# Kernel tuning notes

Measured on AMD Instinct MI355X. Metric: run time of the kernel, lower is better.

## Reference

```python
import jax, jax.numpy as jnp
import numpy as np

B, N, DIN, DM, NH = 8, 2048, 256, 256, 4
DK = DM // NH


def setup_inputs() -> dict:
    key = jax.random.key(0)
    ks = jax.random.split(key, 8)
    x = jax.random.normal(ks[0], (B, N, DIN), dtype=jnp.float32)
    # contiguous valid ranges per sample (padding on both ends), matching
    # the module's assumption that torch.where(mask)[0][0]/[−1] define a span
    starts = jax.random.randint(ks[1], (B,), 0, N // 8)
    lens = jax.random.randint(ks[2], (B,), N // 2, N - N // 8)
    pos = jnp.arange(N)
    attention_mask = ((pos[None, :] >= starts[:, None])
                      & (pos[None, :] < starts[:, None] + lens[:, None])).astype(jnp.int32)
    s = 0.02
    Wq = jax.random.normal(ks[3], (DIN, DM), jnp.float32) * s
    Wk = jax.random.normal(ks[4], (DIN, DM), jnp.float32) * s
    Wv = jax.random.normal(ks[5], (DIN, DM), jnp.float32) * s
    Wo = jax.random.normal(ks[6], (DM, DM), jnp.float32) * s
    bq = jnp.zeros((DM,), jnp.float32)
    bk = jnp.zeros((DM,), jnp.float32)
    bv = jnp.zeros((DM,), jnp.float32)
    bo = jnp.zeros((DM,), jnp.float32)
    return {"x": x, "attention_mask": attention_mask,
            "Wq": Wq, "bq": bq, "Wk": Wk, "bk": bk,
            "Wv": Wv, "bv": bv, "Wo": Wo, "bo": bo}


def reference(x, attention_mask, Wq, bq, Wk, bk, Wv, bv, Wo, bo):
    b, n, _ = x.shape
    nh, dk = NH, DK
    scale = 1.0 / np.sqrt(dk)
    q = (x @ Wq + bq).reshape(b, n, nh, dk).transpose(0, 2, 1, 3)  # [b,h,n,dk]
    k = (x @ Wk + bk).reshape(b, n, nh, dk).transpose(0, 2, 1, 3)
    v = (x @ Wv + bv).reshape(b, n, nh, dk).transpose(0, 2, 1, 3)
    dist = jnp.einsum('bhid,bhjd->bhij', q, k) * scale  # [b,h,n,n]

    # Vectorized equivalent of the per-sample python-loop mask:
    # start = first True index; end = last True index (torch slice start:end
    # is EXCLUSIVE of the last valid position -- preserved faithfully).
    m = attention_mask.astype(bool)
    pos = jnp.arange(n)
    start = jnp.argmax(m, axis=1)                      # [b]
    end = n - 1 - jnp.argmax(m[:, ::-1], axis=1)       # [b] last True index
    valid = (pos[None, :] >= start[:, None]) & (pos[None, :] < end[:, None])  # [b,n]
    bias = jnp.where(valid[:, :, None] & valid[:, None, :], 0.0, -1e10)       # [b,n,n]

    dist = jax.nn.softmax(dist + bias[:, None, :, :], axis=-1)
    att = jnp.einsum('bhij,bhjd->bhid', dist, v)       # [b,h,n,dk]
    att = att.transpose(0, 2, 1, 3).reshape(b, n, nh * dk)
    return att @ Wo + bo
```

## Files before the change

kernel.cpp:

```cpp
#include <hip/hip_runtime.h>
#include <hip/hip_bf16.h>
#include <math.h>

namespace {
constexpr int Bb  = 8;
constexpr int Nn  = 2048;
constexpr int DIN_ = 256;
constexpr int DM_  = 256;
constexpr int NH_  = 4;
constexpr int DK_  = 64;
constexpr int BH_  = Bb * NH_;
constexpr float SCALE = 0.125f;
}

typedef __attribute__((ext_vector_type(8))) _Float16 half8;
typedef __attribute__((ext_vector_type(2))) __fp16 fp16x2;
typedef __attribute__((ext_vector_type(4))) float f32x4;

static __device__ __forceinline__ unsigned pkrtz_u32(float a, float b) {
    union { fp16x2 h; unsigned u; } u;
    u.h = __builtin_amdgcn_cvt_pkrtz(a, b);
    return u.u;
}

static __device__ __forceinline__ half8 h8_from_u32x4(unsigned w0, unsigned w1,
                                                      unsigned w2, unsigned w3) {
    union { unsigned u[4]; half8 h; } u;
    u.u[0] = w0; u.u[1] = w1; u.u[2] = w2; u.u[3] = w3;
    return u.h;
}

__global__ __launch_bounds__(256) void bounds_kernel(const int* __restrict__ mask,
                                                     int* __restrict__ bounds) {
    const int b = blockIdx.x;
    const int tid = threadIdx.x;
    __shared__ int smin[256], smax[256];
    int lmin = Nn, lmax = -1;
    for (int i = tid; i < Nn; i += 256) {
        if (mask[b * Nn + i]) {
            if (i < lmin) lmin = i;
            if (i > lmax) lmax = i;
        }
    }
    smin[tid] = lmin; smax[tid] = lmax;
    __syncthreads();
    for (int s = 128; s > 0; s >>= 1) {
        if (tid < s) {
            smin[tid] = min(smin[tid], smin[tid + s]);
            smax[tid] = max(smax[tid], smax[tid + s]);
        }
        __syncthreads();
    }
    if (tid == 0) { bounds[b * 2] = smin[0]; bounds[b * 2 + 1] = smax[0]; }
}

__global__ __launch_bounds__(256) void convert_x(const float* __restrict__ x,
                                                 _Float16* __restrict__ xh) {
    const size_t i = ((size_t)blockIdx.x * 256 + threadIdx.x) * 8;
    float4 v0 = *(const float4*)&x[i];
    float4 v1 = *(const float4*)&x[i + 4];
    _Float16 h[8];
    h[0]=(_Float16)v0.x; h[1]=(_Float16)v0.y; h[2]=(_Float16)v0.z; h[3]=(_Float16)v0.w;
    h[4]=(_Float16)v1.x; h[5]=(_Float16)v1.y; h[6]=(_Float16)v1.z; h[7]=(_Float16)v1.w;
    *(uint4*)&xh[i] = *(const uint4*)h;
}

__global__ __launch_bounds__(256) void convert_w(
    const float* __restrict__ W0, const float* __restrict__ W1,
    const float* __restrict__ W2, const float* __restrict__ W3,
    _Float16* __restrict__ T0, _Float16* __restrict__ T1,
    _Float16* __restrict__ T2, _Float16* __restrict__ T3)
{
    const float* W; _Float16* T;
    switch (blockIdx.y) {
        case 0: W = W0; T = T0; break;
        case 1: W = W1; T = T1; break;
        case 2: W = W2; T = T2; break;
        default: W = W3; T = T3; break;
    }
    const int idx = blockIdx.x * 256 + threadIdx.x;
    const int n = idx & 255;
    const int k0 = (idx >> 8) << 2;
    _Float16 h4[4];
    #pragma unroll
    for (int j = 0; j < 4; ++j) h4[j] = (_Float16)W[(size_t)(k0 + j) * 256 + n];
    *(uint2*)&T[(size_t)n * 256 + k0] = *(const uint2*)h4;
}

__global__ __launch_bounds__(256) void qkv_mfma(
    const _Float16* __restrict__ xh,
    const _Float16* __restrict__ Wtq, const float* __restrict__ bq,
    const _Float16* __restrict__ Wtk, const float* __restrict__ bk,
    const _Float16* __restrict__ Wtv, const float* __restrict__ bv,
    _Float16* __restrict__ Qh, _Float16* __restrict__ Kh, _Float16* __restrict__ Vt)
{
    const int z = blockIdx.z;
    const _Float16* Wt; const float* bias;
    if (z == 0)      { Wt = Wtq; bias = bq; }
    else if (z == 1) { Wt = Wtk; bias = bk; }
    else             { Wt = Wtv; bias = bv; }

    const int m0 = blockIdx.x * 128;
    const int n0 = blockIdx.y * 64;
    const int tid = threadIdx.x;
    const int w = tid >> 6, lane = tid & 63;
    const int a = lane & 15, g = lane >> 4;
    const int mb = m0 + 32 * w;

    f32x4 d0[4] = {{0,0,0,0},{0,0,0,0},{0,0,0,0},{0,0,0,0}};
    f32x4 d1[4] = {{0,0,0,0},{0,0,0,0},{0,0,0,0},{0,0,0,0}};

    const _Float16* A0 = xh + (size_t)(mb + a) * 256 + 8 * g;
    const _Float16* A1 = xh + (size_t)(mb + 16 + a) * 256 + 8 * g;
    const _Float16* Wr0 = Wt + (size_t)(n0 +  0 + a) * 256 + 8 * g;
    const _Float16* Wr1 = Wt + (size_t)(n0 + 16 + a) * 256 + 8 * g;
    const _Float16* Wr2 = Wt + (size_t)(n0 + 32 + a) * 256 + 8 * g;
    const _Float16* Wr3 = Wt + (size_t)(n0 + 48 + a) * 256 + 8 * g;

    #pragma unroll
    for (int kc = 0; kc < 8; ++kc) {
        const half8 af0 = *(const half8*)(A0 + 32 * kc);
        const half8 af1 = *(const half8*)(A1 + 32 * kc);
        const half8 b0 = *(const half8*)(Wr0 + 32 * kc);
        const half8 b1 = *(const half8*)(Wr1 + 32 * kc);
        const half8 b2 = *(const half8*)(Wr2 + 32 * kc);
        const half8 b3 = *(const half8*)(Wr3 + 32 * kc);
        d0[0] = __builtin_amdgcn_mfma_f32_16x16x32_f16(af0, b0, d0[0], 0,0,0);
        d1[0] = __builtin_amdgcn_mfma_f32_16x16x32_f16(af1, b0, d1[0], 0,0,0);
        d0[1] = __builtin_amdgcn_mfma_f32_16x16x32_f16(af0, b1, d0[1], 0,0,0);
        d1[1] = __builtin_amdgcn_mfma_f32_16x16x32_f16(af1, b1, d1[1], 0,0,0);
        d0[2] = __builtin_amdgcn_mfma_f32_16x16x32_f16(af0, b2, d0[2], 0,0,0);
        d1[2] = __builtin_amdgcn_mfma_f32_16x16x32_f16(af1, b2, d1[2], 0,0,0);
        d0[3] = __builtin_amdgcn_mfma_f32_16x16x32_f16(af0, b3, d0[3], 0,0,0);
        d1[3] = __builtin_amdgcn_mfma_f32_16x16x32_f16(af1, b3, d1[3], 0,0,0);
    }

    #pragma unroll
    for (int t = 0; t < 2; ++t) {
        const int mrow = mb + 16 * t + 4 * g;
        #pragma unroll
        for (int nf = 0; nf < 4; ++nf) {
            const f32x4 dv = t == 0 ? d0[nf] : d1[nf];
            const int n = n0 + 16 * nf + a;
            const float bs = bias[n];
            const int bh = (mrow >> 11) * NH_ + (n >> 6);
            const int dk = n & 63;
            if (z < 2) {
                _Float16* out = z ? Kh : Qh;
                #pragma unroll
                for (int r = 0; r < 4; ++r) {
                    const int tok = (mrow + r) & 2047;
                    out[((size_t)bh * Nn + tok) * DK_ + dk] = (_Float16)(dv[r] + bs);
                }
            } else {
                const int tok = mrow & 2047;
                uint2 pk;
                pk.x = pkrtz_u32(dv[0] + bs, dv[1] + bs);
                pk.y = pkrtz_u32(dv[2] + bs, dv[3] + bs);
                *(uint2*)&Vt[((size_t)bh * DK_ + dk) * Nn + tok] = pk;
            }
        }
    }
}

__global__ __launch_bounds__(256) void colmean_kernel(const _Float16* __restrict__ Vt,
                                                      float* __restrict__ cm) {
    const int bh = blockIdx.x;
    const int t = threadIdx.x;
    const int d = t >> 2, part = t & 3;
    const _Float16* src = Vt + ((size_t)bh * DK_ + d) * Nn + part * 512;
    float s = 0.f;
    for (int i = 0; i < 512; i += 8) {
        half8 v = *(const half8*)(src + i);
        #pragma unroll
        for (int j = 0; j < 8; ++j) s += (float)v[j];
    }
    __shared__ float red[64][4];
    red[d][part] = s;
    __syncthreads();
    if (part == 0)
        cm[bh * DK_ + d] = (red[d][0] + red[d][1] + red[d][2] + red[d][3]) * (1.0f / 2048.0f);
}

__global__ __launch_bounds__(256) void flash_mfma(
    const _Float16* __restrict__ Q, const _Float16* __restrict__ K,
    const _Float16* __restrict__ Vt, const int* __restrict__ bounds,
    const float* __restrict__ cm, _Float16* __restrict__ att)
{
    const int bh = blockIdx.y;
    const int b  = bh >> 2, h = bh & 3;
    const int q0 = blockIdx.x * 64;
    const int tid  = threadIdx.x;
    const int w    = tid >> 6;
    const int lane = tid & 63;
    const int a = lane & 15, g = lane >> 4;
    const int start = bounds[2 * b], endv = bounds[2 * b + 1];

    __shared__ __align__(16) _Float16 kfr[8][512];
    __shared__ __align__(16) _Float16 vfr[8][512];

    const float* cmb = cm + bh * DK_;
    _Float16* attb = att + ((size_t)b * Nn) * DM_ + h * DK_;

    if (q0 + 63 < start || q0 >= endv) {
        #pragma unroll
        for (int td = 0; td < 4; ++td) {
            const _Float16 cmv = (_Float16)cmb[16 * td + a];
            #pragma unroll
            for (int r = 0; r < 4; ++r) {
                const int qr = q0 + 16 * w + 4 * g + r;
                attb[(size_t)qr * DM_ + 16 * td + a] = cmv;
            }
        }
        return;
    }

    const _Float16* Qb = Q  + (size_t)bh * Nn * DK_;
    const _Float16* Kb = K  + (size_t)bh * Nn * DK_;
    const _Float16* Vb = Vt + (size_t)bh * DK_ * Nn;

    const int qrow = q0 + 16 * w + a;
    const half8 qf0 = *(const half8*)&Qb[(size_t)qrow * DK_ + 8 * g];
    const half8 qf1 = *(const half8*)&Qb[(size_t)qrow * DK_ + 32 + 8 * g];

    float l_i = 0.0f;
    f32x4 o0 = {0.f,0.f,0.f,0.f}, o1 = {0.f,0.f,0.f,0.f};
    f32x4 o2 = {0.f,0.f,0.f,0.f}, o3 = {0.f,0.f,0.f,0.f};

    const int lo = (start >> 6) * 64;
    for (int kt = lo; kt < endv; kt += 64) {
        #pragma unroll
        for (int ff = 0; ff < 2; ++ff) {
            const int f  = 2 * w + ff;
            const int tt = f >> 1, c = f & 1;
            const _Float16* ks = &Kb[(size_t)(kt + 16 * tt + a) * DK_ + 32 * c + 8 * g];
            __builtin_amdgcn_global_load_lds(
                (const __attribute__((address_space(1))) void*)ks,
                (__attribute__((address_space(3))) void*)&kfr[f][0], 16, 0, 0);
            const _Float16* vs = &Vb[(size_t)(16 * tt + a) * Nn + kt + 32 * c + 8 * g];
            __builtin_amdgcn_global_load_lds(
                (const __attribute__((address_space(1))) void*)vs,
                (__attribute__((address_space(3))) void*)&vfr[f][0], 16, 0, 0);
        }
        __syncthreads();

        f32x4 st0 = {0.f,0.f,0.f,0.f}, st1 = {0.f,0.f,0.f,0.f};
        f32x4 st2 = {0.f,0.f,0.f,0.f}, st3 = {0.f,0.f,0.f,0.f};
        st0 = __builtin_amdgcn_mfma_f32_16x16x32_f16(*(const half8*)&kfr[0][lane*8], qf0, st0, 0,0,0);
        st0 = __builtin_amdgcn_mfma_f32_16x16x32_f16(*(const half8*)&kfr[1][lane*8], qf1, st0, 0,0,0);
        st1 = __builtin_amdgcn_mfma_f32_16x16x32_f16(*(const half8*)&kfr[2][lane*8], qf0, st1, 0,0,0);
        st1 = __builtin_amdgcn_mfma_f32_16x16x32_f16(*(const half8*)&kfr[3][lane*8], qf1, st1, 0,0,0);
        st2 = __builtin_amdgcn_mfma_f32_16x16x32_f16(*(const half8*)&kfr[4][lane*8], qf0, st2, 0,0,0);
        st2 = __builtin_amdgcn_mfma_f32_16x16x32_f16(*(const half8*)&kfr[5][lane*8], qf1, st2, 0,0,0);
        st3 = __builtin_amdgcn_mfma_f32_16x16x32_f16(*(const half8*)&kfr[6][lane*8], qf0, st3, 0,0,0);
        st3 = __builtin_amdgcn_mfma_f32_16x16x32_f16(*(const half8*)&kfr[7][lane*8], qf1, st3, 0,0,0);

        float pv[4][4];
        float rsum = 0.0f;
        const bool edge = (kt < start) || (kt + 64 > endv);
        if (edge) {
            #pragma unroll
            for (int t = 0; t < 4; ++t) {
                const f32x4 sv = (t == 0) ? st0 : (t == 1) ? st1 : (t == 2) ? st2 : st3;
                #pragma unroll
                for (int r = 0; r < 4; ++r) {
                    const int col = kt + 16 * t + 4 * g + r;
                    const bool ok = (col >= start) && (col < endv);
                    const float e = ok ? __expf(sv[r] * SCALE) : 0.0f;
                    pv[t][r] = e;
                    rsum += e;
                }
            }
        } else {
            #pragma unroll
            for (int t = 0; t < 4; ++t) {
                const f32x4 sv = (t == 0) ? st0 : (t == 1) ? st1 : (t == 2) ? st2 : st3;
                #pragma unroll
                for (int r = 0; r < 4; ++r) {
                    const float e = __expf(sv[r] * SCALE);
                    pv[t][r] = e;
                    rsum += e;
                }
            }
        }
        rsum += __shfl_xor(rsum, 16, 64);
        rsum += __shfl_xor(rsum, 32, 64);
        l_i += rsum;

        unsigned pk[4][2];
        #pragma unroll
        for (int t = 0; t < 4; ++t) {
            pk[t][0] = pkrtz_u32(pv[t][0], pv[t][1]);
            pk[t][1] = pkrtz_u32(pv[t][2], pv[t][3]);
        }
        const int gsel = g >> 1;
        unsigned aw[2][4];
        #pragma unroll
        for (int c = 0; c < 2; ++c) {
            #pragma unroll
            for (int wd = 0; wd < 4; ++wd) {
                const int srcLane = a + 16 * (2 * (g & 1) + (wd >> 1));
                const int lo2 = __shfl((int)pk[2 * c    ][wd & 1], srcLane, 64);
                const int hi2 = __shfl((int)pk[2 * c + 1][wd & 1], srcLane, 64);
                aw[c][wd] = (unsigned)(gsel ? hi2 : lo2);
            }
        }
        const half8 pa0 = h8_from_u32x4(aw[0][0], aw[0][1], aw[0][2], aw[0][3]);
        const half8 pa1 = h8_from_u32x4(aw[1][0], aw[1][1], aw[1][2], aw[1][3]);

        o0 = __builtin_amdgcn_mfma_f32_16x16x32_f16(pa0, *(const half8*)&vfr[0][lane*8], o0, 0,0,0);
        o0 = __builtin_amdgcn_mfma_f32_16x16x32_f16(pa1, *(const half8*)&vfr[1][lane*8], o0, 0,0,0);
        o1 = __builtin_amdgcn_mfma_f32_16x16x32_f16(pa0, *(const half8*)&vfr[2][lane*8], o1, 0,0,0);
        o1 = __builtin_amdgcn_mfma_f32_16x16x32_f16(pa1, *(const half8*)&vfr[3][lane*8], o1, 0,0,0);
        o2 = __builtin_amdgcn_mfma_f32_16x16x32_f16(pa0, *(const half8*)&vfr[4][lane*8], o2, 0,0,0);
        o2 = __builtin_amdgcn_mfma_f32_16x16x32_f16(pa1, *(const half8*)&vfr[5][lane*8], o2, 0,0,0);
        o3 = __builtin_amdgcn_mfma_f32_16x16x32_f16(pa0, *(const half8*)&vfr[6][lane*8], o3, 0,0,0);
        o3 = __builtin_amdgcn_mfma_f32_16x16x32_f16(pa1, *(const half8*)&vfr[7][lane*8], o3, 0,0,0);

        __syncthreads();
    }

    const float inv = 1.0f / l_i;
    const float ir0 = __shfl(inv, 4 * g + 0, 64);
    const float ir1 = __shfl(inv, 4 * g + 1, 64);
    const float ir2 = __shfl(inv, 4 * g + 2, 64);
    const float ir3 = __shfl(inv, 4 * g + 3, 64);

    #pragma unroll
    for (int td = 0; td < 4; ++td) {
        const f32x4 ov = (td == 0) ? o0 : (td == 1) ? o1 : (td == 2) ? o2 : o3;
        const float cmv = cmb[16 * td + a];
        const float irs[4] = {ir0, ir1, ir2, ir3};
        #pragma unroll
        for (int r = 0; r < 4; ++r) {
            const int qr = q0 + 16 * w + 4 * g + r;
            const bool valid = (qr >= start) && (qr < endv);
            const float val = valid ? ov[r] * irs[r] : cmv;
            attb[(size_t)qr * DM_ + 16 * td + a] = (_Float16)val;
        }
    }
}

__global__ __launch_bounds__(256) void proj_mfma(
    const _Float16* __restrict__ A, const _Float16* __restrict__ Wt,
    const float* __restrict__ bias, float* __restrict__ out)
{
    const int m0 = blockIdx.x * 128;
    const int n0 = blockIdx.y * 64;
    const int tid = threadIdx.x;
    const int w = tid >> 6, lane = tid & 63;
    const int a = lane & 15, g = lane >> 4;
    const int mb = m0 + 32 * w;

    f32x4 d0[4] = {{0,0,0,0},{0,0,0,0},{0,0,0,0},{0,0,0,0}};
    f32x4 d1[4] = {{0,0,0,0},{0,0,0,0},{0,0,0,0},{0,0,0,0}};

    const _Float16* A0 = A + (size_t)(mb + a) * 256 + 8 * g;
    const _Float16* A1 = A + (size_t)(mb + 16 + a) * 256 + 8 * g;
    const _Float16* Wr0 = Wt + (size_t)(n0 +  0 + a) * 256 + 8 * g;
    const _Float16* Wr1 = Wt + (size_t)(n0 + 16 + a) * 256 + 8 * g;
    const _Float16* Wr2 = Wt + (size_t)(n0 + 32 + a) * 256 + 8 * g;
    const _Float16* Wr3 = Wt + (size_t)(n0 + 48 + a) * 256 + 8 * g;

    #pragma unroll
    for (int kc = 0; kc < 8; ++kc) {
        const half8 af0 = *(const half8*)(A0 + 32 * kc);
        const half8 af1 = *(const half8*)(A1 + 32 * kc);
        const half8 b0 = *(const half8*)(Wr0 + 32 * kc);
        const half8 b1 = *(const half8*)(Wr1 + 32 * kc);
        const half8 b2 = *(const half8*)(Wr2 + 32 * kc);
        const half8 b3 = *(const half8*)(Wr3 + 32 * kc);
        d0[0] = __builtin_amdgcn_mfma_f32_16x16x32_f16(af0, b0, d0[0], 0,0,0);
        d1[0] = __builtin_amdgcn_mfma_f32_16x16x32_f16(af1, b0, d1[0], 0,0,0);
        d0[1] = __builtin_amdgcn_mfma_f32_16x16x32_f16(af0, b1, d0[1], 0,0,0);
        d1[1] = __builtin_amdgcn_mfma_f32_16x16x32_f16(af1, b1, d1[1], 0,0,0);
        d0[2] = __builtin_amdgcn_mfma_f32_16x16x32_f16(af0, b2, d0[2], 0,0,0);
        d1[2] = __builtin_amdgcn_mfma_f32_16x16x32_f16(af1, b2, d1[2], 0,0,0);
        d0[3] = __builtin_amdgcn_mfma_f32_16x16x32_f16(af0, b3, d0[3], 0,0,0);
        d1[3] = __builtin_amdgcn_mfma_f32_16x16x32_f16(af1, b3, d1[3], 0,0,0);
    }

    #pragma unroll
    for (int t = 0; t < 2; ++t) {
        const int mrow = mb + 16 * t + 4 * g;
        #pragma unroll
        for (int nf = 0; nf < 4; ++nf) {
            const f32x4 dv = t == 0 ? d0[nf] : d1[nf];
            const int n = n0 + 16 * nf + a;
            const float bs = bias[n];
            #pragma unroll
            for (int r = 0; r < 4; ++r)
                out[(size_t)(mrow + r) * DM_ + n] = dv[r] + bs;
        }
    }
}

extern "C" void kernel_launch(void* const* d_in, const int* in_sizes, int n_in,
                              void* d_out, int out_size, void* d_ws, size_t ws_size,
                              hipStream_t stream)
{
    const float* x    = (const float*)d_in[0];
    const int*   mask = (const int*)d_in[1];
    const float* Wq   = (const float*)d_in[2];
    const float* bq   = (const float*)d_in[3];
    const float* Wk   = (const float*)d_in[4];
    const float* bk   = (const float*)d_in[5];
    const float* Wv   = (const float*)d_in[6];
    const float* bv   = (const float*)d_in[7];
    const float* Wo   = (const float*)d_in[8];
    const float* bo   = (const float*)d_in[9];
    float* out = (float*)d_out;

    char* ws = (char*)d_ws;
    size_t off = 0;
    int* bounds = (int*)ws;                 off += 256;
    float* cmv  = (float*)(ws + off);       off += (size_t)BH_ * DK_ * sizeof(float);
    off = (off + 255) & ~(size_t)255;
    const size_t h16_bytes = (size_t)BH_ * Nn * DK_ * sizeof(_Float16);
    _Float16* xh  = (_Float16*)(ws + off); off += h16_bytes;
    _Float16* Qh  = (_Float16*)(ws + off); off += h16_bytes;
    _Float16* Kh  = (_Float16*)(ws + off); off += h16_bytes;
    _Float16* Vt  = (_Float16*)(ws + off); off += h16_bytes;
    _Float16* ath = (_Float16*)(ws + off); off += h16_bytes;
    _Float16* Wtq = (_Float16*)(ws + off); off += 256 * 256 * sizeof(_Float16);
    _Float16* Wtk = (_Float16*)(ws + off); off += 256 * 256 * sizeof(_Float16);
    _Float16* Wtv = (_Float16*)(ws + off); off += 256 * 256 * sizeof(_Float16);
    _Float16* Wto = (_Float16*)(ws + off); off += 256 * 256 * sizeof(_Float16);

    bounds_kernel<<<Bb, 256, 0, stream>>>(mask, bounds);
    convert_x<<<2048, 256, 0, stream>>>(x, xh);
    convert_w<<<dim3(64, 4), 256, 0, stream>>>(Wq, Wk, Wv, Wo, Wtq, Wtk, Wtv, Wto);

    dim3 g1(Bb * Nn / 128, DM_ / 64, 3);
    qkv_mfma<<<g1, 256, 0, stream>>>(xh, Wtq, bq, Wtk, bk, Wtv, bv, Qh, Kh, Vt);

    colmean_kernel<<<BH_, 256, 0, stream>>>(Vt, cmv);

    dim3 g2(Nn / 64, BH_);
    flash_mfma<<<g2, 256, 0, stream>>>(Qh, Kh, Vt, bounds, cmv, ath);

    dim3 g3(Bb * Nn / 128, DM_ / 64);
    proj_mfma<<<g3, 256, 0, stream>>>(ath, Wto, bo, out);
}
```

Before: 207.1 us.

## Double-buffer K/V tiles in flash kernel, remap blocks per XCD, merge prep kernels

Three changes. The flash attention loop now double-buffers its K/V LDS tiles: it prefetches the next tile with async global-to-LDS loads while computing the current one, and uses explicit vmcnt waits and raw barriers in place of __syncthreads. The flash grid is flattened to 1D and remapped so that all query blocks of the same four heads (one batch) land on the same XCD, which is meant to improve L2 reuse of K/V. The bounds, x-conversion and weight-conversion kernels are merged into one launch to cut launch overhead. The cost is doubled LDS use per block, which may lower occupancy, and reliance on hand-placed waitcnt counts being correct.

```diff
diff --git a/kernel.cpp b/kernel.cpp
--- a/kernel.cpp
+++ b/kernel.cpp
@@ -30,61 +30,62 @@
     return u.h;
 }
 
-__global__ __launch_bounds__(256) void bounds_kernel(const int* __restrict__ mask,
-                                                     int* __restrict__ bounds) {
-    const int b = blockIdx.x;
-    const int tid = threadIdx.x;
-    __shared__ int smin[256], smax[256];
-    int lmin = Nn, lmax = -1;
-    for (int i = tid; i < Nn; i += 256) {
-        if (mask[b * Nn + i]) {
-            if (i < lmin) lmin = i;
-            if (i > lmax) lmax = i;
-        }
-    }
-    smin[tid] = lmin; smax[tid] = lmax;
-    __syncthreads();
-    for (int s = 128; s > 0; s >>= 1) {
-        if (tid < s) {
-            smin[tid] = min(smin[tid], smin[tid + s]);
-            smax[tid] = max(smax[tid], smax[tid + s]);
-        }
-        __syncthreads();
-    }
-    if (tid == 0) { bounds[b * 2] = smin[0]; bounds[b * 2 + 1] = smax[0]; }
-}
-
-__global__ __launch_bounds__(256) void convert_x(const float* __restrict__ x,
-                                                 _Float16* __restrict__ xh) {
-    const size_t i = ((size_t)blockIdx.x * 256 + threadIdx.x) * 8;
-    float4 v0 = *(const float4*)&x[i];
-    float4 v1 = *(const float4*)&x[i + 4];
-    _Float16 h[8];
-    h[0]=(_Float16)v0.x; h[1]=(_Float16)v0.y; h[2]=(_Float16)v0.z; h[3]=(_Float16)v0.w;
-    h[4]=(_Float16)v1.x; h[5]=(_Float16)v1.y; h[6]=(_Float16)v1.z; h[7]=(_Float16)v1.w;
-    *(uint4*)&xh[i] = *(const uint4*)h;
-}
-
-__global__ __launch_bounds__(256) void convert_w(
+__global__ __launch_bounds__(256) void prep_kernel(
+    const int* __restrict__ mask, int* __restrict__ bounds,
+    const float* __restrict__ x, _Float16* __restrict__ xh,
     const float* __restrict__ W0, const float* __restrict__ W1,
     const float* __restrict__ W2, const float* __restrict__ W3,
     _Float16* __restrict__ T0, _Float16* __restrict__ T1,
     _Float16* __restrict__ T2, _Float16* __restrict__ T3)
 {
-    const float* W; _Float16* T;
-    switch (blockIdx.y) {
-        case 0: W = W0; T = T0; break;
-        case 1: W = W1; T = T1; break;
-        case 2: W = W2; T = T2; break;
-        default: W = W3; T = T3; break;
-    }
-    const int idx = blockIdx.x * 256 + threadIdx.x;
-    const int n = idx & 255;
-    const int k0 = (idx >> 8) << 2;
-    _Float16 h4[4];
-    #pragma unroll
-    for (int j = 0; j < 4; ++j) h4[j] = (_Float16)W[(size_t)(k0 + j) * 256 + n];
-    *(uint2*)&T[(size_t)n * 256 + k0] = *(const uint2*)h4;
+    const int bid = blockIdx.x;
+    const int tid = threadIdx.x;
+    if (bid < 8) {
+        const int b = bid;
+        __shared__ int smin[256], smax[256];
+        int lmin = Nn, lmax = -1;
+        for (int i = tid; i < Nn; i += 256) {
+            if (mask[b * Nn + i]) {
+                if (i < lmin) lmin = i;
+                if (i > lmax) lmax = i;
+            }
+        }
+        smin[tid] = lmin; smax[tid] = lmax;
+        __syncthreads();
+        for (int s = 128; s > 0; s >>= 1) {
+            if (tid < s) {
+                smin[tid] = min(smin[tid], smin[tid + s]);
+                smax[tid] = max(smax[tid], smax[tid + s]);
+            }
+            __syncthreads();
+        }
+        if (tid == 0) { bounds[b * 2] = smin[0]; bounds[b * 2 + 1] = smax[0]; }
+    } else if (bid < 8 + 2048) {
+        const size_t i = ((size_t)(bid - 8) * 256 + tid) * 8;
+        float4 v0 = *(const float4*)&x[i];
+        float4 v1 = *(const float4*)&x[i + 4];
+        _Float16 h[8];
+        h[0]=(_Float16)v0.x; h[1]=(_Float16)v0.y; h[2]=(_Float16)v0.z; h[3]=(_Float16)v0.w;
+        h[4]=(_Float16)v1.x; h[5]=(_Float16)v1.y; h[6]=(_Float16)v1.z; h[7]=(_Float16)v1.w;
+        *(uint4*)&xh[i] = *(const uint4*)h;
+    } else {
+        const int lin = bid - 2056;
+        const int wsel = lin >> 6;
+        const float* W; _Float16* T;
+        switch (wsel) {
+            case 0: W = W0; T = T0; break;
+            case 1: W = W1; T = T1; break;
+            case 2: W = W2; T = T2; break;
+            default: W = W3; T = T3; break;
+        }
+        const int idx = (lin & 63) * 256 + tid;
+        const int n = idx & 255;
+        const int k0 = (idx >> 8) << 2;
+        _Float16 h4[4];
+        #pragma unroll
+        for (int j = 0; j < 4; ++j) h4[j] = (_Float16)W[(size_t)(k0 + j) * 256 + n];
+        *(uint2*)&T[(size_t)n * 256 + k0] = *(const uint2*)h4;
+    }
 }
 
 __global__ __launch_bounds__(256) void qkv_mfma(
@@ -187,17 +188,21 @@
     const _Float16* __restrict__ Vt, const int* __restrict__ bounds,
     const float* __restrict__ cm, _Float16* __restrict__ att)
 {
-    const int bh = blockIdx.y;
+    const int bid = blockIdx.x;
+    const int xcd = bid & 7;
+    const int rest = bid >> 3;
+    const int qb  = rest & 31;
+    const int bh  = (xcd << 2) | (rest >> 5);
     const int b  = bh >> 2, h = bh & 3;
-    const int q0 = blockIdx.x * 64;
+    const int q0 = qb * 64;
     const int tid  = threadIdx.x;
     const int w    = tid >> 6;
     const int lane = tid & 63;
     const int a = lane & 15, g = lane >> 4;
     const int start = bounds[2 * b], endv = bounds[2 * b + 1];
 
-    __shared__ __align__(16) _Float16 kfr[8][512];
-    __shared__ __align__(16) _Float16 vfr[8][512];
+    __shared__ __align__(16) _Float16 kfr[2][8][512];
+    __shared__ __align__(16) _Float16 vfr[2][8][512];
 
     const float* cmb = cm + bh * DK_;
     _Float16* attb = att + ((size_t)b * Nn) * DM_ + h * DK_;
@@ -227,33 +232,49 @@
     f32x4 o0 = {0.f,0.f,0.f,0.f}, o1 = {0.f,0.f,0.f,0.f};
     f32x4 o2 = {0.f,0.f,0.f,0.f}, o3 = {0.f,0.f,0.f,0.f};
 
+#define STAGE(cbuf, kt_) do {                                                        \
+        _Pragma("unroll")                                                            \
+        for (int ff = 0; ff < 2; ++ff) {                                             \
+            const int f  = 2 * w + ff;                                               \
+            const int tt = f >> 1, cc = f & 1;                                       \
+            const _Float16* ks = &Kb[(size_t)((kt_) + 16 * tt + a) * DK_ + 32 * cc + 8 * g]; \
+            __builtin_amdgcn_global_load_lds(                                        \
+                (const __attribute__((address_space(1))) void*)ks,                   \
+                (__attribute__((address_space(3))) void*)&kfr[cbuf][f][0], 16, 0, 0);\
+            const _Float16* vs = &Vb[(size_t)(16 * tt + a) * Nn + (kt_) + 32 * cc + 8 * g]; \
+            __builtin_amdgcn_global_load_lds(                                        \
+                (const __attribute__((address_space(1))) void*)vs,                   \
+                (__attribute__((address_space(3))) void*)&vfr[cbuf][f][0], 16, 0, 0);\
+        }                                                                            \
+    } while (0)
+
     const int lo = (start >> 6) * 64;
+    int c = 0;
+    STAGE(0, lo);
+
     for (int kt = lo; kt < endv; kt += 64) {
-        #pragma unroll
-        for (int ff = 0; ff < 2; ++ff) {
-            const int f  = 2 * w + ff;
-            const int tt = f >> 1, c = f & 1;
-            const _Float16* ks = &Kb[(size_t)(kt + 16 * tt + a) * DK_ + 32 * c + 8 * g];
-            __builtin_amdgcn_global_load_lds(
-                (const __attribute__((address_space(1))) void*)ks,
-                (__attribute__((address_space(3))) void*)&kfr[f][0], 16, 0, 0);
-            const _Float16* vs = &Vb[(size_t)(16 * tt + a) * Nn + kt + 32 * c + 8 * g];
-            __builtin_amdgcn_global_load_lds(
-                (const __attribute__((address_space(1))) void*)vs,
-                (__attribute__((address_space(3))) void*)&vfr[f][0], 16, 0, 0);
-        }
-        __syncthreads();
+        const int nxt = kt + 64;
+        if (nxt < endv) {
+            STAGE(c ^ 1, nxt);
+            asm volatile("s_waitcnt vmcnt(4)" ::: "memory");
+        } else {
+            asm volatile("s_waitcnt vmcnt(0)" ::: "memory");
+        }
+        __builtin_amdgcn_s_barrier();
+
+        const _Float16* kf = &kfr[c][0][0];
+        const _Float16* vf = &vfr[c][0][0];
 
         f32x4 st0 = {0.f,0.f,0.f,0.f}, st1 = {0.f,0.f,0.f,0.f};
         f32x4 st2 = {0.f,0.f,0.f,0.f}, st3 = {0.f,0.f,0.f,0.f};
-        st0 = __builtin_amdgcn_mfma_f32_16x16x32_f16(*(const half8*)&kfr[0][lane*8], qf0, st0, 0,0,0);
-        st0 = __builtin_amdgcn_mfma_f32_16x16x32_f16(*(const half8*)&kfr[1][lane*8], qf1, st0, 0,0,0);
-        st1 = __builtin_amdgcn_mfma_f32_16x16x32_f16(*(const half8*)&kfr[2][lane*8], qf0, st1, 0,0,0);
-        st1 = __builtin_amdgcn_mfma_f32_16x16x32_f16(*(const half8*)&kfr[3][lane*8], qf1, st1, 0,0,0);
-        st2 = __builtin_amdgcn_mfma_f32_16x16x32_f16(*(const half8*)&kfr[4][lane*8], qf0, st2, 0,0,0);
-        st2 = __builtin_amdgcn_mfma_f32_16x16x32_f16(*(const half8*)&kfr[5][lane*8], qf1, st2, 0,0,0);
-        st3 = __builtin_amdgcn_mfma_f32_16x16x32_f16(*(const half8*)&kfr[6][lane*8], qf0, st3, 0,0,0);
-        st3 = __builtin_amdgcn_mfma_f32_16x16x32_f16(*(const half8*)&kfr[7][lane*8], qf1, st3, 0,0,0);
+        st0 = __builtin_amdgcn_mfma_f32_16x16x32_f16(*(const half8*)&kf[0*512 + lane*8], qf0, st0, 0,0,0);
+        st0 = __builtin_amdgcn_mfma_f32_16x16x32_f16(*(const half8*)&kf[1*512 + lane*8], qf1, st0, 0,0,0);
+        st1 = __builtin_amdgcn_mfma_f32_16x16x32_f16(*(const half8*)&kf[2*512 + lane*8], qf0, st1, 0,0,0);
+        st1 = __builtin_amdgcn_mfma_f32_16x16x32_f16(*(const half8*)&kf[3*512 + lane*8], qf1, st1, 0,0,0);
+        st2 = __builtin_amdgcn_mfma_f32_16x16x32_f16(*(const half8*)&kf[4*512 + lane*8], qf0, st2, 0,0,0);
+        st2 = __builtin_amdgcn_mfma_f32_16x16x32_f16(*(const half8*)&kf[5*512 + lane*8], qf1, st2, 0,0,0);
+        st3 = __builtin_amdgcn_mfma_f32_16x16x32_f16(*(const half8*)&kf[6*512 + lane*8], qf0, st3, 0,0,0);
+        st3 = __builtin_amdgcn_mfma_f32_16x16x32_f16(*(const half8*)&kf[7*512 + lane*8], qf1, st3, 0,0,0);
 
         float pv[4][4];
         float rsum = 0.0f;
@@ -296,29 +317,32 @@
         const int gsel = g >> 1;
         unsigned aw[2][4];
         #pragma unroll
-        for (int c = 0; c < 2; ++c) {
+        for (int cq = 0; cq < 2; ++cq) {
             #pragma unroll
             for (int wd = 0; wd < 4; ++wd) {
                 const int srcLane = a + 16 * (2 * (g & 1) + (wd >> 1));
-                const int lo2 = __shfl((int)pk[2 * c    ][wd & 1], srcLane, 64);
-                const int hi2 = __shfl((int)pk[2 * c + 1][wd & 1], srcLane, 64);
-                aw[c][wd] = (unsigned)(gsel ? hi2 : lo2);
+                const int lo2 = __shfl((int)pk[2 * cq    ][wd & 1], srcLane, 64);
+                const int hi2 = __shfl((int)pk[2 * cq + 1][wd & 1], srcLane, 64);
+                aw[cq][wd] = (unsigned)(gsel ? hi2 : lo2);
             }
         }
         const half8 pa0 = h8_from_u32x4(aw[0][0], aw[0][1], aw[0][2], aw[0][3]);
         const half8 pa1 = h8_from_u32x4(aw[1][0], aw[1][1], aw[1][2], aw[1][3]);
 
-        o0 = __builtin_amdgcn_mfma_f32_16x16x32_f16(pa0, *(const half8*)&vfr[0][lane*8], o0, 0,0,0);
-        o0 = __builtin_amdgcn_mfma_f32_16x16x32_f16(pa1, *(const half8*)&vfr[1][lane*8], o0, 0,0,0);
-        o1 = __builtin_amdgcn_mfma_f32_16x16x32_f16(pa0, *(const half8*)&vfr[2][lane*8], o1, 0,0,0);
-        o1 = __builtin_amdgcn_mfma_f32_16x16x32_f16(pa1, *(const half8*)&vfr[3][lane*8], o1, 0,0,0);
-        o2 = __builtin_amdgcn_mfma_f32_16x16x32_f16(pa0, *(const half8*)&vfr[4][lane*8], o2, 0,0,0);
-        o2 = __builtin_amdgcn_mfma_f32_16x16x32_f16(pa1, *(const half8*)&vfr[5][lane*8], o2, 0,0,0);
-        o3 = __builtin_amdgcn_mfma_f32_16x16x32_f16(pa0, *(const half8*)&vfr[6][lane*8], o3, 0,0,0);
-        o3 = __builtin_amdgcn_mfma_f32_16x16x32_f16(pa1, *(const half8*)&vfr[7][lane*8], o3, 0,0,0);
-
-        __syncthreads();
-    }
+        o0 = __builtin_amdgcn_mfma_f32_16x16x32_f16(pa0, *(const half8*)&vf[0*512 + lane*8], o0, 0,0,0);
+        o0 = __builtin_amdgcn_mfma_f32_16x16x32_f16(pa1, *(const half8*)&vf[1*512 + lane*8], o0, 0,0,0);
+        o1 = __builtin_amdgcn_mfma_f32_16x16x32_f16(pa0, *(const half8*)&vf[2*512 + lane*8], o1, 0,0,0);
+        o1 = __builtin_amdgcn_mfma_f32_16x16x32_f16(pa1, *(const half8*)&vf[3*512 + lane*8], o1, 0,0,0);
+        o2 = __builtin_amdgcn_mfma_f32_16x16x32_f16(pa0, *(const half8*)&vf[4*512 + lane*8], o2, 0,0,0);
+        o2 = __builtin_amdgcn_mfma_f32_16x16x32_f16(pa1, *(const half8*)&vf[5*512 + lane*8], o2, 0,0,0);
+        o3 = __builtin_amdgcn_mfma_f32_16x16x32_f16(pa0, *(const half8*)&vf[6*512 + lane*8], o3, 0,0,0);
+        o3 = __builtin_amdgcn_mfma_f32_16x16x32_f16(pa1, *(const half8*)&vf[7*512 + lane*8], o3, 0,0,0);
+
+        asm volatile("" ::: "memory");
+        __builtin_amdgcn_s_barrier();
+        c ^= 1;
+    }
+#undef STAGE
 
     const float inv = 1.0f / l_i;
     const float ir0 = __shfl(inv, 4 * g + 0, 64);
@@ -427,17 +451,15 @@
     _Float16* Wtv = (_Float16*)(ws + off); off += 256 * 256 * sizeof(_Float16);
     _Float16* Wto = (_Float16*)(ws + off); off += 256 * 256 * sizeof(_Float16);
 
-    bounds_kernel<<<Bb, 256, 0, stream>>>(mask, bounds);
-    convert_x<<<2048, 256, 0, stream>>>(x, xh);
-    convert_w<<<dim3(64, 4), 256, 0, stream>>>(Wq, Wk, Wv, Wo, Wtq, Wtk, Wtv, Wto);
+    prep_kernel<<<2312, 256, 0, stream>>>(mask, bounds, x, xh,
+                                          Wq, Wk, Wv, Wo, Wtq, Wtk, Wtv, Wto);
 
     dim3 g1(Bb * Nn / 128, DM_ / 64, 3);
     qkv_mfma<<<g1, 256, 0, stream>>>(xh, Wtq, bq, Wtk, bk, Wtv, bv, Qh, Kh, Vt);
 
     colmean_kernel<<<BH_, 256, 0, stream>>>(Vt, cmv);
 
-    dim3 g2(Nn / 64, BH_);
-    flash_mfma<<<g2, 256, 0, stream>>>(Qh, Kh, Vt, bounds, cmv, ath);
+    flash_mfma<<<1024, 256, 0, stream>>>(Qh, Kh, Vt, bounds, cmv, ath);
 
     dim3 g3(Bb * Nn / 128, DM_ / 64);
     proj_mfma<<<g3, 256, 0, stream>>>(ath, Wto, bo, out);
```

Measured after the change: 208.9 us. Within noise of the previous version (+0.9%).
